# Performance work log

Measured on AMD Instinct MI355X. Metric: run time of the kernel, lower is better.

Reference implementation:

```python
import jax, jax.numpy as jnp
import numpy as np

THRESH = 1.0   # firing threshold used in forward1 (IF_Neuron(..., 1.0))
EPS = 1e-5     # spike detection epsilon from SpikingNN
T_NORM = 256.0 # hard-coded divisor in forward1
GAMMA = 1.0 / 2.2

# SpikingNN: forward is a hard 0/1 spike, backward is a straight-through
# pass gated on ex_membrane > EPS (matches the torch autograd.Function).
@jax.custom_vjp
def spike(ex):
    return (ex > EPS).astype(ex.dtype)

def _spike_fwd(ex):
    return (ex > EPS).astype(ex.dtype), (ex > EPS)

def _spike_bwd(mask, g):
    return (jnp.where(mask, g, 0.0),)

spike.defvjp(_spike_fwd, _spike_bwd)

def _sif_forward(x):
    # x: [T, H, W, C]; sequential IF-neuron integrate/fire scan over T.
    def step(mem, xt):
        mem = mem + xt
        # torch F.threshold(mem, thr, 0): mem where mem > thr else 0;
        # its grad passes only where mem > thr (jnp.where matches this).
        ex = jnp.where(mem > THRESH, mem, jnp.zeros_like(mem))
        mem = mem - ex  # soft reset: subtract the excess membrane
        s = spike(ex)
        # out = s.detach() + (1/thr)*s - (1/thr)*s.detach()
        # value == s; grad w.r.t. s scaled by 1/thr (straight-through trick)
        sg = jax.lax.stop_gradient(s)
        out = sg + (1.0 / THRESH) * s - (1.0 / THRESH) * sg
        return mem, out

    mem0 = jnp.zeros(x.shape[1:], dtype=x.dtype)
    _, outs = jax.lax.scan(step, mem0, x)  # outs: [T, H, W, C]
    y = jnp.sum(outs, axis=0) / T_NORM
    return y ** GAMMA  # gamma correction, pow(y, 1/2.2)

def setup_inputs() -> dict:
    key = jax.random.key(0)
    # uniform [0,1) spike-camera-like intensities so the IF neuron fires
    x = jax.random.uniform(key, (256, 256, 256, 3), dtype=jnp.float32)
    return {"x": x}

def reference(x):
    return _sif_forward(x)
```

## Files before the change

### kernel.cpp

```cpp
#include <hip/hip_runtime.h>
#include <math.h>


#define T_STEPS 256
#define NPIX (256 * 256 * 3)
#define NV (NPIX / 4)
#define PF 8

__device__ __forceinline__ void sif_step(float4& mem, float4& cnt, float4 v) {
    mem.x += v.x; mem.y += v.y; mem.z += v.z; mem.w += v.w;
    bool fx = mem.x > 1.0f, fy = mem.y > 1.0f, fz = mem.z > 1.0f, fw = mem.w > 1.0f;
    cnt.x += fx ? 1.0f : 0.0f; cnt.y += fy ? 1.0f : 0.0f;
    cnt.z += fz ? 1.0f : 0.0f; cnt.w += fw ? 1.0f : 0.0f;
    mem.x = fx ? 0.0f : mem.x; mem.y = fy ? 0.0f : mem.y;
    mem.z = fz ? 0.0f : mem.z; mem.w = fw ? 0.0f : mem.w;
}

__global__ __launch_bounds__(64) void sif_kernel(const float* __restrict__ x,
                                                 float* __restrict__ out) {
    const int gid = blockIdx.x * blockDim.x + threadIdx.x;
    const float4* __restrict__ p = reinterpret_cast<const float4*>(x) + gid;

    float4 mem = make_float4(0.f, 0.f, 0.f, 0.f);
    float4 cnt = make_float4(0.f, 0.f, 0.f, 0.f);

    float4 a[PF], b[PF];

#pragma unroll
    for (int k = 0; k < PF; ++k) a[k] = p[k * NV];

    for (int tb = 0; tb < T_STEPS / PF; ++tb) {
        if (tb + 1 < T_STEPS / PF) {
            const int base = (tb + 1) * PF;
#pragma unroll
            for (int k = 0; k < PF; ++k) b[k] = p[(base + k) * NV];
        }
#pragma unroll
        for (int k = 0; k < PF; ++k) sif_step(mem, cnt, a[k]);
#pragma unroll
        for (int k = 0; k < PF; ++k) a[k] = b[k];
    }

    const float g = 1.0f / 2.2f;
    float4 r;
    r.x = powf(cnt.x * (1.0f / 256.0f), g);
    r.y = powf(cnt.y * (1.0f / 256.0f), g);
    r.z = powf(cnt.z * (1.0f / 256.0f), g);
    r.w = powf(cnt.w * (1.0f / 256.0f), g);
    reinterpret_cast<float4*>(out)[gid] = r;
}

extern "C" void kernel_launch(void* const* d_in, const int* in_sizes, int n_in,
                              void* d_out, int out_size, void* d_ws, size_t ws_size,
                              hipStream_t stream) {
    const float* x = (const float*)d_in[0];
    float* out = (float*)d_out;

    const int threads = 64;
    const int blocks = NV / threads;
    sif_kernel<<<blocks, threads, 0, stream>>>(x, out);
}
```

Measured before the change: 261.9 us.

## Process four float4 columns per thread with a rolling per-step prefetch buffer

Each thread now integrates four float4 pixel groups instead of one, so the grid shrinks fourfold. The batch prefetch with a copy step is replaced by a rolling buffer: each slot is refilled with the load for step t+DEPTH as soon as it is consumed, aiming to keep a steady number of loads in flight. The goal is to hide the memory latency of this strided streaming scan. In exchange, the grid drops to 192 single-wave blocks, fewer than the CU count, so some CUs may sit idle, and register pressure rises with the 32-entry buffer.

```diff
diff --git a/kernel.cpp b/kernel.cpp
--- a/kernel.cpp
+++ b/kernel.cpp
@@ -5,7 +5,8 @@
 #define T_STEPS 256
 #define NPIX (256 * 256 * 3)
 #define NV (NPIX / 4)
-#define PF 8
+#define PPT 4
+#define DEPTH 8
 
 __device__ __forceinline__ void sif_step(float4& mem, float4& cnt, float4 v) {
     mem.x += v.x; mem.y += v.y; mem.z += v.z; mem.w += v.w;
@@ -18,36 +19,54 @@
 
 __global__ __launch_bounds__(64) void sif_kernel(const float* __restrict__ x,
                                                  float* __restrict__ out) {
-    const int gid = blockIdx.x * blockDim.x + threadIdx.x;
-    const float4* __restrict__ p = reinterpret_cast<const float4*>(x) + gid;
+    const int base = blockIdx.x * (64 * PPT) + threadIdx.x;
+    const float4* __restrict__ p = reinterpret_cast<const float4*>(x) + base;
 
-    float4 mem = make_float4(0.f, 0.f, 0.f, 0.f);
-    float4 cnt = make_float4(0.f, 0.f, 0.f, 0.f);
+    float4 mem[PPT], cnt[PPT];
+#pragma unroll
+    for (int j = 0; j < PPT; ++j) {
+        mem[j] = make_float4(0.f, 0.f, 0.f, 0.f);
+        cnt[j] = make_float4(0.f, 0.f, 0.f, 0.f);
+    }
 
-    float4 a[PF], b[PF];
+    float4 buf[DEPTH][PPT];
 
 #pragma unroll
-    for (int k = 0; k < PF; ++k) a[k] = p[k * NV];
+    for (int d = 0; d < DEPTH; ++d)
+#pragma unroll
+        for (int j = 0; j < PPT; ++j)
+            buf[d][j] = p[d * NV + j * 64];
 
-    for (int tb = 0; tb < T_STEPS / PF; ++tb) {
-        if (tb + 1 < T_STEPS / PF) {
-            const int base = (tb + 1) * PF;
+    for (int tb = 0; tb < T_STEPS / DEPTH - 1; ++tb) {
 #pragma unroll
-            for (int k = 0; k < PF; ++k) b[k] = p[(base + k) * NV];
+        for (int d = 0; d < DEPTH; ++d) {
+            const int tnext = tb * DEPTH + d + DEPTH;
+#pragma unroll
+            for (int j = 0; j < PPT; ++j) {
+                float4 v = buf[d][j];
+                buf[d][j] = p[tnext * NV + j * 64];
+                sif_step(mem[j], cnt[j], v);
+            }
         }
-#pragma unroll
-        for (int k = 0; k < PF; ++k) sif_step(mem, cnt, a[k]);
-#pragma unroll
-        for (int k = 0; k < PF; ++k) a[k] = b[k];
     }
 
+#pragma unroll
+    for (int d = 0; d < DEPTH; ++d)
+#pragma unroll
+        for (int j = 0; j < PPT; ++j)
+            sif_step(mem[j], cnt[j], buf[d][j]);
+
     const float g = 1.0f / 2.2f;
-    float4 r;
-    r.x = powf(cnt.x * (1.0f / 256.0f), g);
-    r.y = powf(cnt.y * (1.0f / 256.0f), g);
-    r.z = powf(cnt.z * (1.0f / 256.0f), g);
-    r.w = powf(cnt.w * (1.0f / 256.0f), g);
-    reinterpret_cast<float4*>(out)[gid] = r;
+    float4* o = reinterpret_cast<float4*>(out) + base;
+#pragma unroll
+    for (int j = 0; j < PPT; ++j) {
+        float4 r;
+        r.x = powf(cnt[j].x * (1.0f / 256.0f), g);
+        r.y = powf(cnt[j].y * (1.0f / 256.0f), g);
+        r.z = powf(cnt[j].z * (1.0f / 256.0f), g);
+        r.w = powf(cnt[j].w * (1.0f / 256.0f), g);
+        o[j * 64] = r;
+    }
 }
 
 extern "C" void kernel_launch(void* const* d_in, const int* in_sizes, int n_in,
@@ -57,6 +76,6 @@
     float* out = (float*)d_out;
 
     const int threads = 64;
-    const int blocks = NV / threads;
+    const int blocks = NV / (threads * PPT);
     sif_kernel<<<blocks, threads, 0, stream>>>(x, out);
 }
```

After: 268.9 us. 1.03x slower.
